# Kernel optimization log

Hardware: AMD Instinct MI355X
Metric: run time of the kernel (lower is better)

## Reference

```python
import jax, jax.numpy as jnp
import numpy as np

N = 65536
H = 512
E = 8
OUT = 2

def setup_inputs() -> dict:
    key = jax.random.key(0)
    ks = jax.random.split(key, 9)
    s = 0.1
    return {
        "x": jax.random.normal(ks[0], (N, 10), dtype=jnp.float32),
        "w1": jax.random.normal(ks[1], (H,), dtype=jnp.float32) * s,        # fc1: Linear(1,H) weight
        "b1": jax.random.normal(ks[2], (H,), dtype=jnp.float32) * s,
        "meta_w": jax.random.normal(ks[3], (E, H), dtype=jnp.float32) * s,  # 8 Linear(1,H) weights stacked
        "meta_b": jax.random.normal(ks[4], (E, H), dtype=jnp.float32) * s,
        "w2": jax.random.normal(ks[5], (H, H), dtype=jnp.float32) * s,      # fc2 weight (in,out layout)
        "b2": jax.random.normal(ks[6], (H,), dtype=jnp.float32) * s,
        "w3": jax.random.normal(ks[7], (H, OUT), dtype=jnp.float32) * s,    # fc3 weight
        "b3": jax.random.normal(ks[8], (OUT,), dtype=jnp.float32) * s,
    }

def reference(x, w1, b1, meta_w, meta_b, w2, b2, w3, b3):
    one_hot = x[:, 0:8]          # [N,8] expert combine weights
    delta = x[:, 8:9]            # [N,1]
    phi = x[:, 9:10]             # [N,1]
    # fc1(delta): Linear with input_dim=1 -> outer product with weight column
    x1 = delta * w1[None, :] + b1[None, :]                       # [N,H]
    # Per-expert Linear(1,H) on phi, combined with one_hot. Since each expert
    # is linear in phi, the dense [N,H,8] tensor + matmul of the original
    # collapses exactly to: phi * (one_hot @ meta_w) + one_hot @ meta_b.
    x2 = phi * (one_hot @ meta_w) + one_hot @ meta_b             # [N,H]
    h = jax.nn.relu(x1 + x2)
    h = jax.nn.relu(h @ w2 + b2)
    return h @ w3 + b3                                           # [N,OUT]
```

## Files before the change

kernel.cpp:

```cpp
#include <hip/hip_runtime.h>


#define BM 64

typedef float f32x4 __attribute__((ext_vector_type(4)));
typedef short s16x8 __attribute__((ext_vector_type(8)));

__device__ __forceinline__ short f2bf(float f) {
    union { float f; unsigned u; } c; c.f = f;
    unsigned u = c.u;
    return (short)((u + 0x7FFFu + ((u >> 16) & 1u)) >> 16);
}

__global__ void prep_kernel(const float* __restrict__ w1, const float* __restrict__ b1,
                            const float* __restrict__ mw, const float* __restrict__ mb,
                            const float* __restrict__ w2,
                            short* __restrict__ w2s, short* __restrict__ waugS) {
    int id = blockIdx.x * 256 + threadIdx.x;
    if (id < 512 * 512) {
        int k = id / 512, n = id % 512;
        int ks = k >> 5, g = (k >> 3) & 3, j = k & 7;
        w2s[(((ks * 4 + g) * 512) + n) * 8 + j] = f2bf(w2[id]);
    }
    if (id < 512 * 32) {
        int col = id >> 5, k = id & 31;
        float v = 0.f;
        if (k < 8)        v = mw[k * 512 + col];
        else if (k < 16)  v = mb[(k - 8) * 512 + col];
        else if (k == 16) v = w1[col];
        else if (k == 17) v = b1[col];
        waugS[col * 32 + k] = f2bf(v);
    }
}

__global__ __launch_bounds__(512, 4) void fused_mlp(
    const float* __restrict__ x, const short* __restrict__ waugS,
    const short* __restrict__ w2s, const float* __restrict__ b2,
    const float* __restrict__ w3, const float* __restrict__ b3,
    float* __restrict__ out) {

    __shared__ __align__(16) short haug[64 * 512];
    __shared__ float xls[64 * 10];
    __shared__ float oacc[128];

    const int tid  = threadIdx.x;
    const int wv   = tid >> 6;
    const int lane = tid & 63;
    const int l15  = lane & 15;
    const int g    = lane >> 4;
    const long rowbase = (long)blockIdx.x * BM;

    for (int i = tid; i < BM * 10; i += 512) xls[i] = x[rowbase * 10 + i];
    if (tid < 128) oacc[tid] = 0.f;
    __syncthreads();

    {
        s16x8 afr[4];
#pragma unroll
        for (int m = 0; m < 4; ++m) {
            int r = m * 16 + l15;
            float v[8];
            if (g == 0) {
                float phi = xls[r * 10 + 9];
#pragma unroll
                for (int j = 0; j < 8; ++j) v[j] = xls[r * 10 + j] * phi;
            } else if (g == 1) {
#pragma unroll
                for (int j = 0; j < 8; ++j) v[j] = xls[r * 10 + j];
            } else if (g == 2) {
                v[0] = xls[r * 10 + 8]; v[1] = 1.f;
#pragma unroll
                for (int j = 2; j < 8; ++j) v[j] = 0.f;
            } else {
#pragma unroll
                for (int j = 0; j < 8; ++j) v[j] = 0.f;
            }
            s16x8 a;
#pragma unroll
            for (int j = 0; j < 8; ++j) a[j] = f2bf(v[j]);
            afr[m] = a;
        }
#pragma unroll
        for (int nf = 0; nf < 4; ++nf) {
            int col = wv * 64 + nf * 16 + l15;
            s16x8 bfr = *(const s16x8*)(waugS + col * 32 + g * 8);
            int chi = (col >> 3) * 512 + (col & 7);
#pragma unroll
            for (int m = 0; m < 4; ++m) {
                f32x4 c = {0.f, 0.f, 0.f, 0.f};
                c = __builtin_amdgcn_mfma_f32_16x16x32_bf16(afr[m], bfr, c, 0, 0, 0);
#pragma unroll
                for (int r4 = 0; r4 < 4; ++r4) {
                    int row = m * 16 + g * 4 + r4;
                    float hv = c[r4];
                    hv = hv > 0.f ? hv : 0.f;
                    haug[chi + row * 8] = f2bf(hv);
                }
            }
        }
    }
    __syncthreads();

    f32x4 acc[4][4];
#pragma unroll
    for (int m = 0; m < 4; ++m)
#pragma unroll
        for (int n = 0; n < 4; ++n) acc[m][n] = (f32x4){0.f, 0.f, 0.f, 0.f};

    const char* bfp = (const char*)w2s + (g * 512 + wv * 64 + l15) * 16;
    const char* hbp = (const char*)haug + g * 1024 + l15 * 16;

#pragma unroll 1
    for (int t = 0; t < 16; ++t) {
        s16x8 bf0 = *(const s16x8*)(bfp);
        s16x8 bf1 = *(const s16x8*)(bfp + 256);
        s16x8 bf2 = *(const s16x8*)(bfp + 512);
        s16x8 bf3 = *(const s16x8*)(bfp + 768);
        s16x8 a0  = *(const s16x8*)(hbp);
        s16x8 a1  = *(const s16x8*)(hbp + 256);
        acc[0][0] = __builtin_amdgcn_mfma_f32_16x16x32_bf16(a0, bf0, acc[0][0], 0, 0, 0);
        acc[0][1] = __builtin_amdgcn_mfma_f32_16x16x32_bf16(a0, bf1, acc[0][1], 0, 0, 0);
        acc[0][2] = __builtin_amdgcn_mfma_f32_16x16x32_bf16(a0, bf2, acc[0][2], 0, 0, 0);
        acc[0][3] = __builtin_amdgcn_mfma_f32_16x16x32_bf16(a0, bf3, acc[0][3], 0, 0, 0);
        acc[1][0] = __builtin_amdgcn_mfma_f32_16x16x32_bf16(a1, bf0, acc[1][0], 0, 0, 0);
        acc[1][1] = __builtin_amdgcn_mfma_f32_16x16x32_bf16(a1, bf1, acc[1][1], 0, 0, 0);
        acc[1][2] = __builtin_amdgcn_mfma_f32_16x16x32_bf16(a1, bf2, acc[1][2], 0, 0, 0);
        acc[1][3] = __builtin_amdgcn_mfma_f32_16x16x32_bf16(a1, bf3, acc[1][3], 0, 0, 0);
        __builtin_amdgcn_sched_barrier(0);
        s16x8 a2  = *(const s16x8*)(hbp + 512);
        s16x8 a3  = *(const s16x8*)(hbp + 768);
        acc[2][0] = __builtin_amdgcn_mfma_f32_16x16x32_bf16(a2, bf0, acc[2][0], 0, 0, 0);
        acc[2][1] = __builtin_amdgcn_mfma_f32_16x16x32_bf16(a2, bf1, acc[2][1], 0, 0, 0);
        acc[2][2] = __builtin_amdgcn_mfma_f32_16x16x32_bf16(a2, bf2, acc[2][2], 0, 0, 0);
        acc[2][3] = __builtin_amdgcn_mfma_f32_16x16x32_bf16(a2, bf3, acc[2][3], 0, 0, 0);
        acc[3][0] = __builtin_amdgcn_mfma_f32_16x16x32_bf16(a3, bf0, acc[3][0], 0, 0, 0);
        acc[3][1] = __builtin_amdgcn_mfma_f32_16x16x32_bf16(a3, bf1, acc[3][1], 0, 0, 0);
        acc[3][2] = __builtin_amdgcn_mfma_f32_16x16x32_bf16(a3, bf2, acc[3][2], 0, 0, 0);
        acc[3][3] = __builtin_amdgcn_mfma_f32_16x16x32_bf16(a3, bf3, acc[3][3], 0, 0, 0);
        bfp += 32768;
        hbp += 4096;
    }

    float bb2[4], w30[4], w31[4];
#pragma unroll
    for (int n = 0; n < 4; ++n) {
        int col = wv * 64 + n * 16 + l15;
        bb2[n] = b2[col];
        w30[n] = w3[col * 2 + 0];
        w31[n] = w3[col * 2 + 1];
    }
#pragma unroll
    for (int m = 0; m < 4; ++m) {
#pragma unroll
        for (int r4 = 0; r4 < 4; ++r4) {
            float s0 = 0.f, s1 = 0.f;
#pragma unroll
            for (int n = 0; n < 4; ++n) {
                float v = acc[m][n][r4] + bb2[n];
                v = v > 0.f ? v : 0.f;
                s0 += v * w30[n];
                s1 += v * w31[n];
            }
            s0 += __shfl_xor(s0, 1); s1 += __shfl_xor(s1, 1);
            s0 += __shfl_xor(s0, 2); s1 += __shfl_xor(s1, 2);
            s0 += __shfl_xor(s0, 4); s1 += __shfl_xor(s1, 4);
            s0 += __shfl_xor(s0, 8); s1 += __shfl_xor(s1, 8);
            if (l15 == 0) {
                int row = m * 16 + g * 4 + r4;
                atomicAdd(&oacc[row * 2 + 0], s0);
                atomicAdd(&oacc[row * 2 + 1], s1);
            }
        }
    }
    __syncthreads();

    if (tid < 128) {
        int row = tid >> 1, o = tid & 1;
        out[(rowbase + row) * 2 + o] = oacc[tid] + b3[o];
    }
}

extern "C" void kernel_launch(void* const* d_in, const int* in_sizes, int n_in,
                              void* d_out, int out_size, void* d_ws, size_t ws_size,
                              hipStream_t stream) {
    const float* x  = (const float*)d_in[0];
    const float* w1 = (const float*)d_in[1];
    const float* b1 = (const float*)d_in[2];
    const float* mw = (const float*)d_in[3];
    const float* mb = (const float*)d_in[4];
    const float* w2 = (const float*)d_in[5];
    const float* b2 = (const float*)d_in[6];
    const float* w3 = (const float*)d_in[7];
    const float* b3 = (const float*)d_in[8];
    float* out = (float*)d_out;

    short* w2s   = (short*)d_ws;
    short* waugS = w2s + 512 * 512;

    prep_kernel<<<1024, 256, 0, stream>>>(w1, b1, mw, mb, w2, w2s, waugS);
    fused_mlp<<<65536 / BM, 512, 0, stream>>>(x, waugS, w2s, b2, w3, b3, out);
}
```

Before: 53.94 us.

## Double row tile to 128 with 1024-thread blocks and 32-column warp slices

Raises the rows per block from 64 to 128 and the block size to 1024 threads (16 waves), and gives each wave 32 output columns instead of 64. Each w2 fragment fetched from global memory is now reused across 8 row fragments instead of 4, which halves w2 traffic per row. The cost is twice the LDS per block (128 KB for the hidden activations), so fewer blocks fit per CU, and half as many blocks are launched. The per-wave accumulator count is unchanged.

```diff
diff --git a/kernel.cpp b/kernel.cpp
--- a/kernel.cpp
+++ b/kernel.cpp
@@ -1,7 +1,7 @@
 #include <hip/hip_runtime.h>
 
 
-#define BM 64
+#define BM 128
 
 typedef float f32x4 __attribute__((ext_vector_type(4)));
 typedef short s16x8 __attribute__((ext_vector_type(8)));
@@ -33,15 +33,15 @@
     }
 }
 
-__global__ __launch_bounds__(512, 4) void fused_mlp(
+__global__ __launch_bounds__(1024, 4) void fused_mlp(
     const float* __restrict__ x, const short* __restrict__ waugS,
     const short* __restrict__ w2s, const float* __restrict__ b2,
     const float* __restrict__ w3, const float* __restrict__ b3,
     float* __restrict__ out) {
 
-    __shared__ __align__(16) short haug[64 * 512];
-    __shared__ float xls[64 * 10];
-    __shared__ float oacc[128];
+    __shared__ __align__(16) short haug[128 * 512];
+    __shared__ float xls[128 * 10];
+    __shared__ float oacc[256];
 
     const int tid  = threadIdx.x;
     const int wv   = tid >> 6;
@@ -50,14 +50,19 @@
     const int g    = lane >> 4;
     const long rowbase = (long)blockIdx.x * BM;
 
-    for (int i = tid; i < BM * 10; i += 512) xls[i] = x[rowbase * 10 + i];
-    if (tid < 128) oacc[tid] = 0.f;
+    for (int i = tid; i < BM * 10; i += 1024) xls[i] = x[rowbase * 10 + i];
+    if (tid < 256) oacc[tid] = 0.f;
     __syncthreads();
 
     {
-        s16x8 afr[4];
-#pragma unroll
-        for (int m = 0; m < 4; ++m) {
+        s16x8 bfr[2];
+#pragma unroll
+        for (int nf = 0; nf < 2; ++nf) {
+            int col = wv * 32 + nf * 16 + l15;
+            bfr[nf] = *(const s16x8*)(waugS + col * 32 + g * 8);
+        }
+#pragma unroll
+        for (int m = 0; m < 8; ++m) {
             int r = m * 16 + l15;
             float v[8];
             if (g == 0) {
@@ -78,17 +83,12 @@
             s16x8 a;
 #pragma unroll
             for (int j = 0; j < 8; ++j) a[j] = f2bf(v[j]);
-            afr[m] = a;
-        }
-#pragma unroll
-        for (int nf = 0; nf < 4; ++nf) {
-            int col = wv * 64 + nf * 16 + l15;
-            s16x8 bfr = *(const s16x8*)(waugS + col * 32 + g * 8);
-            int chi = (col >> 3) * 512 + (col & 7);
-#pragma unroll
-            for (int m = 0; m < 4; ++m) {
+#pragma unroll
+            for (int nf = 0; nf < 2; ++nf) {
+                int col = wv * 32 + nf * 16 + l15;
+                int chi = (col >> 3) * 1024 + (col & 7);
                 f32x4 c = {0.f, 0.f, 0.f, 0.f};
-                c = __builtin_amdgcn_mfma_f32_16x16x32_bf16(afr[m], bfr, c, 0, 0, 0);
+                c = __builtin_amdgcn_mfma_f32_16x16x32_bf16(a, bfr[nf], c, 0, 0, 0);
 #pragma unroll
                 for (int r4 = 0; r4 < 4; ++r4) {
                     int row = m * 16 + g * 4 + r4;
@@ -101,61 +101,63 @@
     }
     __syncthreads();
 
-    f32x4 acc[4][4];
-#pragma unroll
-    for (int m = 0; m < 4; ++m)
-#pragma unroll
-        for (int n = 0; n < 4; ++n) acc[m][n] = (f32x4){0.f, 0.f, 0.f, 0.f};
-
-    const char* bfp = (const char*)w2s + (g * 512 + wv * 64 + l15) * 16;
-    const char* hbp = (const char*)haug + g * 1024 + l15 * 16;
+    f32x4 acc[8][2];
+#pragma unroll
+    for (int m = 0; m < 8; ++m)
+#pragma unroll
+        for (int n = 0; n < 2; ++n) acc[m][n] = (f32x4){0.f, 0.f, 0.f, 0.f};
+
+    const char* bfp = (const char*)w2s + g * 8192 + (wv * 32 + l15) * 16;
+    const char* hbp = (const char*)haug + g * 2048 + l15 * 16;
 
 #pragma unroll 1
     for (int t = 0; t < 16; ++t) {
         s16x8 bf0 = *(const s16x8*)(bfp);
         s16x8 bf1 = *(const s16x8*)(bfp + 256);
-        s16x8 bf2 = *(const s16x8*)(bfp + 512);
-        s16x8 bf3 = *(const s16x8*)(bfp + 768);
         s16x8 a0  = *(const s16x8*)(hbp);
         s16x8 a1  = *(const s16x8*)(hbp + 256);
+        s16x8 a2  = *(const s16x8*)(hbp + 512);
+        s16x8 a3  = *(const s16x8*)(hbp + 768);
         acc[0][0] = __builtin_amdgcn_mfma_f32_16x16x32_bf16(a0, bf0, acc[0][0], 0, 0, 0);
         acc[0][1] = __builtin_amdgcn_mfma_f32_16x16x32_bf16(a0, bf1, acc[0][1], 0, 0, 0);
-        acc[0][2] = __builtin_amdgcn_mfma_f32_16x16x32_bf16(a0, bf2, acc[0][2], 0, 0, 0);
-        acc[0][3] = __builtin_amdgcn_mfma_f32_16x16x32_bf16(a0, bf3, acc[0][3], 0, 0, 0);
         acc[1][0] = __builtin_amdgcn_mfma_f32_16x16x32_bf16(a1, bf0, acc[1][0], 0, 0, 0);
         acc[1][1] = __builtin_amdgcn_mfma_f32_16x16x32_bf16(a1, bf1, acc[1][1], 0, 0, 0);
-        acc[1][2] = __builtin_amdgcn_mfma_f32_16x16x32_bf16(a1, bf2, acc[1][2], 0, 0, 0);
-        acc[1][3] = __builtin_amdgcn_mfma_f32_16x16x32_bf16(a1, bf3, acc[1][3], 0, 0, 0);
-        __builtin_amdgcn_sched_barrier(0);
-        s16x8 a2  = *(const s16x8*)(hbp + 512);
-        s16x8 a3  = *(const s16x8*)(hbp + 768);
         acc[2][0] = __builtin_amdgcn_mfma_f32_16x16x32_bf16(a2, bf0, acc[2][0], 0, 0, 0);
         acc[2][1] = __builtin_amdgcn_mfma_f32_16x16x32_bf16(a2, bf1, acc[2][1], 0, 0, 0);
-        acc[2][2] = __builtin_amdgcn_mfma_f32_16x16x32_bf16(a2, bf2, acc[2][2], 0, 0, 0);
-        acc[2][3] = __builtin_amdgcn_mfma_f32_16x16x32_bf16(a2, bf3, acc[2][3], 0, 0, 0);
         acc[3][0] = __builtin_amdgcn_mfma_f32_16x16x32_bf16(a3, bf0, acc[3][0], 0, 0, 0);
         acc[3][1] = __builtin_amdgcn_mfma_f32_16x16x32_bf16(a3, bf1, acc[3][1], 0, 0, 0);
-        acc[3][2] = __builtin_amdgcn_mfma_f32_16x16x32_bf16(a3, bf2, acc[3][2], 0, 0, 0);
-        acc[3][3] = __builtin_amdgcn_mfma_f32_16x16x32_bf16(a3, bf3, acc[3][3], 0, 0, 0);
+        __builtin_amdgcn_sched_barrier(0);
+        s16x8 a4  = *(const s16x8*)(hbp + 1024);
+        s16x8 a5  = *(const s16x8*)(hbp + 1280);
+        s16x8 a6  = *(const s16x8*)(hbp + 1536);
+        s16x8 a7  = *(const s16x8*)(hbp + 1792);
+        acc[4][0] = __builtin_amdgcn_mfma_f32_16x16x32_bf16(a4, bf0, acc[4][0], 0, 0, 0);
+        acc[4][1] = __builtin_amdgcn_mfma_f32_16x16x32_bf16(a4, bf1, acc[4][1], 0, 0, 0);
+        acc[5][0] = __builtin_amdgcn_mfma_f32_16x16x32_bf16(a5, bf0, acc[5][0], 0, 0, 0);
+        acc[5][1] = __builtin_amdgcn_mfma_f32_16x16x32_bf16(a5, bf1, acc[5][1], 0, 0, 0);
+        acc[6][0] = __builtin_amdgcn_mfma_f32_16x16x32_bf16(a6, bf0, acc[6][0], 0, 0, 0);
+        acc[6][1] = __builtin_amdgcn_mfma_f32_16x16x32_bf16(a6, bf1, acc[6][1], 0, 0, 0);
+        acc[7][0] = __builtin_amdgcn_mfma_f32_16x16x32_bf16(a7, bf0, acc[7][0], 0, 0, 0);
+        acc[7][1] = __builtin_amdgcn_mfma_f32_16x16x32_bf16(a7, bf1, acc[7][1], 0, 0, 0);
         bfp += 32768;
-        hbp += 4096;
-    }
-
-    float bb2[4], w30[4], w31[4];
-#pragma unroll
-    for (int n = 0; n < 4; ++n) {
-        int col = wv * 64 + n * 16 + l15;
+        hbp += 8192;
+    }
+
+    float bb2[2], w30[2], w31[2];
+#pragma unroll
+    for (int n = 0; n < 2; ++n) {
+        int col = wv * 32 + n * 16 + l15;
         bb2[n] = b2[col];
         w30[n] = w3[col * 2 + 0];
         w31[n] = w3[col * 2 + 1];
     }
 #pragma unroll
-    for (int m = 0; m < 4; ++m) {
+    for (int m = 0; m < 8; ++m) {
 #pragma unroll
         for (int r4 = 0; r4 < 4; ++r4) {
             float s0 = 0.f, s1 = 0.f;
 #pragma unroll
-            for (int n = 0; n < 4; ++n) {
+            for (int n = 0; n < 2; ++n) {
                 float v = acc[m][n][r4] + bb2[n];
                 v = v > 0.f ? v : 0.f;
                 s0 += v * w30[n];
@@ -174,7 +176,7 @@
     }
     __syncthreads();
 
-    if (tid < 128) {
+    if (tid < 256) {
         int row = tid >> 1, o = tid & 1;
         out[(rowbase + row) * 2 + o] = oacc[tid] + b3[o];
     }
@@ -198,5 +200,5 @@
     short* waugS = w2s + 512 * 512;
 
     prep_kernel<<<1024, 256, 0, stream>>>(w1, b1, mw, mb, w2, w2s, waugS);
-    fused_mlp<<<65536 / BM, 512, 0, stream>>>(x, waugS, w2s, b2, w3, b3, out);
-}
+    fused_mlp<<<65536 / BM, 1024, 0, stream>>>(x, waugS, w2s, b2, w3, b3, out);
+}
```

Result: slower. 73.34 us (+36.0%).
